# Kernel optimization log

Hardware: AMD Instinct MI355X
Metric: run time of the kernel (lower is better)

The kernel has to match this reference:

```python
import jax, jax.numpy as jnp
import numpy as np

UP = 16  # up_scale
EPS = 1e-5


def conv2d(x, w, b, pad):
    # x: [N,C,H,W], w: [O,I,kh,kw]
    out = jax.lax.conv_general_dilated(
        x, w, window_strides=(1, 1), padding=[(pad, pad), (pad, pad)],
        dimension_numbers=("NCHW", "OIHW", "NCHW"))
    return out + b[None, :, None, None]


def batchnorm(x, gamma, beta):
    # torch BatchNorm2d training mode: biased batch stats over (N,H,W)
    mu = jnp.mean(x, axis=(0, 2, 3), keepdims=True)
    var = jnp.var(x, axis=(0, 2, 3), keepdims=True)
    xn = (x - mu) * jax.lax.rsqrt(var + EPS)
    return xn * gamma[None, :, None, None] + beta[None, :, None, None]


def unfold3x3(x):
    # F.unfold(x, [3,3], padding=1) -> [N, C, 9, H, W] with (kh,kw) row-major order
    N, C, H, W = x.shape
    xp = jnp.pad(x, ((0, 0), (0, 0), (1, 1), (1, 1)))
    patches = [xp[:, :, i:i + H, j:j + W] for i in range(3) for j in range(3)]
    return jnp.stack(patches, axis=2)


def setup_inputs() -> dict:
    key = jax.random.key(0)
    ks = jax.random.split(key, 14)
    N, Cin, H, W = 4, 128, 64, 64
    Cout = 2
    s = 0.05
    inp = {
        "img_f": jax.random.normal(ks[0], (N, Cin, H, W), jnp.float32),
        # flowhead: conv3x3 -> BN -> ReLU -> conv3x3
        "fh_w1": jax.random.normal(ks[1], (Cout, Cin, 3, 3), jnp.float32) * s,
        "fh_b1": jax.random.normal(ks[2], (Cout,), jnp.float32) * s,
        "fh_g": jnp.ones((Cout,), jnp.float32),
        "fh_beta": jnp.zeros((Cout,), jnp.float32),
        "fh_w2": jax.random.normal(ks[3], (Cout, Cout, 3, 3), jnp.float32) * s,
        "fh_b2": jax.random.normal(ks[4], (Cout,), jnp.float32) * s,
        # mask head: conv3x3 -> BN -> ReLU -> conv1x1
        "mk_w1": jax.random.normal(ks[5], (UP * UP, Cin, 3, 3), jnp.float32) * s,
        "mk_b1": jax.random.normal(ks[6], (UP * UP,), jnp.float32) * s,
        "mk_g": jnp.ones((UP * UP,), jnp.float32),
        "mk_beta": jnp.zeros((UP * UP,), jnp.float32),
        "mk_w2": jax.random.normal(ks[7], (UP * UP * 9, UP * UP, 1, 1), jnp.float32) * s,
        "mk_b2": jax.random.normal(ks[8], (UP * UP * 9,), jnp.float32) * s,
    }
    return inp


def reference(img_f, fh_w1, fh_b1, fh_g, fh_beta, fh_w2, fh_b2,
              mk_w1, mk_b1, mk_g, mk_beta, mk_w2, mk_b2):
    # flow head
    h = conv2d(img_f, fh_w1, fh_b1, pad=1)
    h = jax.nn.relu(batchnorm(h, fh_g, fh_beta))
    flow = conv2d(h, fh_w2, fh_b2, pad=1)          # [N, C, H, W]

    # mask head
    m = conv2d(img_f, mk_w1, mk_b1, pad=1)
    m = jax.nn.relu(batchnorm(m, mk_g, mk_beta))
    mask = conv2d(m, mk_w2, mk_b2, pad=0) * 0.25   # [N, 9*UP*UP, H, W]

    N, C, H, W = flow.shape
    mask = mask.reshape(N, 1, 9, UP, UP, H, W)
    mask = jax.nn.softmax(mask, axis=2)

    up_flow = unfold3x3(8.0 * flow)                # [N, C, 9, H, W]
    up_flow = up_flow[:, :, :, None, None, :, :]   # [N, C, 9, 1, 1, H, W]
    up_flow = jnp.sum(mask * up_flow, axis=2)      # [N, C, UP, UP, H, W]
    up_flow = jnp.transpose(up_flow, (0, 1, 4, 2, 5, 3))  # [N, C, H, UP, W, UP]
    return up_flow.reshape(N, C, UP * H, UP * W)
```

## Files before the change

### kernel.cpp

```cpp
#include <hip/hip_runtime.h>
#include <hip/hip_bf16.h>

#define N_B   4
#define C_IN  128
#define HWSZ  4096
#define C_M   256

typedef __attribute__((ext_vector_type(8))) short          s16x8;
typedef __attribute__((ext_vector_type(8))) unsigned short u16x8;
typedef __attribute__((ext_vector_type(4))) unsigned short u16x4;
typedef __attribute__((ext_vector_type(4))) float          f32x4;

__device__ __forceinline__ unsigned short f2bf(float f) {
    union { float f; unsigned u; } v; v.f = f;
    unsigned r = v.u + 0x7fffu + ((v.u >> 16) & 1u);
    return (unsigned short)(r >> 16);
}
__device__ __forceinline__ float bf2f(unsigned short u) {
    union { unsigned u; float f; } v; v.u = ((unsigned)u) << 16; return v.f;
}

__global__ void __launch_bounds__(256)
prep_all(const float* __restrict__ img,
         const float* __restrict__ mk_w1, const float* __restrict__ fh_w1,
         const float* __restrict__ mk_w2,
         unsigned short* __restrict__ imgT,
         unsigned short* __restrict__ w1f, unsigned short* __restrict__ w2f)
{
    __shared__ float s[128][65];
    const int b = blockIdx.x;
    if (b < 256) {
        const int n = b >> 6, h = b & 63;
        const float* src = img + (size_t)n * C_IN * HWSZ + h * 64;
        for (int i = threadIdx.x; i < 128 * 64; i += 256) {
            int ci = i >> 6, w = i & 63;
            s[ci][w] = src[(size_t)ci * HWSZ + w];
        }
        __syncthreads();
        unsigned short* dst = imgT + ((size_t)(n * 64 + h) * 64) * 128;
        for (int i = threadIdx.x; i < 64 * 128; i += 256) {
            int w = i >> 7, ci = i & 127;
            dst[(size_t)w * 128 + ci] = f2bf(s[ci][w]);
        }
        return;
    }
    int i = (b - 256) * 256 + threadIdx.x;
    if (i < 2304 * 256) {
        int uvt = i / 36864;
        int r   = i - uvt * 36864;
        int k   = r / 4096;
        int r2  = r - k * 4096;
        int ks  = r2 >> 9;
        int lg  = (r2 >> 7) & 3;
        int ln  = (r2 >> 3) & 15;
        int j   = r2 & 7;
        w2f[i] = f2bf(0.25f * mk_w2[(size_t)(k * 256 + uvt * 16 + ln) * 256 + ks * 32 + lg * 8 + j]);
    }
    if (i < 2 * 4 * 9 * 9 * 512) {
        int z   = i / 165888;
        int r   = i - z * 165888;
        int cc  = r / 41472;
        int r2  = r - cc * 41472;
        int tap = r2 / 4608;
        int r3  = r2 - tap * 4608;
        int g   = r3 / 512;
        int r4  = r3 - g * 512;
        int lane = r4 >> 3, j = r4 & 7;
        int lg = lane >> 4, ln = lane & 15;
        int row = g * 16 + ln;
        int ci  = cc * 32 + lg * 8 + j;
        float w = 0.f;
        if (z == 0) {
            if (row < 128)      w = mk_w1[((size_t)row * C_IN + ci) * 9 + tap];
            else if (row < 130) w = fh_w1[((size_t)(row - 128) * C_IN + ci) * 9 + tap];
        } else {
            if (row < 128)      w = mk_w1[((size_t)(128 + row) * C_IN + ci) * 9 + tap];
        }
        w1f[i] = f2bf(w);
    }
}

__global__ void __launch_bounds__(512, 4)
conv1_mfma(const unsigned short* __restrict__ imgT,
           const unsigned short* __restrict__ w1f,
           const float* __restrict__ mk_b1, const float* __restrict__ fh_b1,
           unsigned short* __restrict__ m_frag, float* __restrict__ h_pre,
           float* __restrict__ ps_s, float* __restrict__ ps_s2)
{
    __shared__ unsigned short s_img[3][66][40];
    __shared__ float s_bias[144];
    __shared__ float s_ps[2][144], s_ps2[2][144];

    const int hw = blockIdx.x;
    const int xcd = hw & 7, slot = hw >> 3;
    const int lid = xcd * 64 + slot;
    const int n = lid >> 7, h = (lid >> 1) & 63, z = lid & 1;
    const int hn = n * 64 + h;

    const int tid = threadIdx.x;
    const int wv = tid >> 6, lane = tid & 63;
    const int lg = lane >> 4, ln = lane & 15;
    const int gq = wv >> 1, half = wv & 1;
    const int g0 = z ? (gq * 2) : ((int[4]){0, 3, 5, 7})[gq];
    const int gn = z ? 2 : ((int[4]){3, 2, 2, 2})[gq];

    if (tid < 144) {
        float b = 0.f;
        if (z == 0) {
            if (tid < 128)      b = mk_b1[tid];
            else if (tid < 130) b = fh_b1[tid - 128];
        } else if (tid < 128)   b = mk_b1[128 + tid];
        s_bias[tid] = b;
    }

    f32x4 acc[3][2];
#pragma unroll
    for (int g = 0; g < 3; ++g)
#pragma unroll
        for (int q = 0; q < 2; ++q) acc[g][q] = (f32x4){0.f, 0.f, 0.f, 0.f};

    for (int cc = 0; cc < 4; ++cc) {
        __syncthreads();
        for (int i = tid; i < 3 * 66 * 4; i += 512) {
            int r = i / 264;
            int rem = i - r * 264;
            int c = rem >> 2, un = rem & 3;
            int gy = h - 1 + r, gx = c - 1;
            u16x8 v = {0, 0, 0, 0, 0, 0, 0, 0};
            if ((unsigned)gy < 64u && (unsigned)gx < 64u)
                v = *(const u16x8*)&imgT[((size_t)((n * 64 + gy) * 64 + gx)) * 128 + cc * 32 + un * 8];
            *(u16x8*)&s_img[r][c][un * 8] = v;
        }
        __syncthreads();

        const unsigned short* wfp = w1f + (size_t)(z * 4 + cc) * 81 * 512 + lane * 8;
#pragma unroll
        for (int tap = 0; tap < 9; ++tap) {
            const int dy = tap / 3, dx = tap % 3;
            s16x8 bf[2];
#pragma unroll
            for (int q = 0; q < 2; ++q)
                bf[q] = *(const s16x8*)&s_img[dy][half * 32 + q * 16 + ln + dx][lg * 8];
#pragma unroll
            for (int gi = 0; gi < 3; ++gi) {
                if (gi < gn) {
                    s16x8 af = *(const s16x8*)&wfp[(size_t)(tap * 9 + g0 + gi) * 512];
#pragma unroll
                    for (int q = 0; q < 2; ++q)
                        acc[gi][q] = __builtin_amdgcn_mfma_f32_16x16x32_bf16(af, bf[q], acc[gi][q], 0, 0, 0);
                }
            }
        }
    }

#pragma unroll
    for (int gi = 0; gi < 3; ++gi) {
        if (gi >= gn) continue;
        const int g = g0 + gi;
        float v[2][4];
#pragma unroll
        for (int q = 0; q < 2; ++q)
#pragma unroll
            for (int r = 0; r < 4; ++r)
                v[q][r] = acc[gi][q][r] + s_bias[g * 16 + lg * 4 + r];
#pragma unroll
        for (int q = 0; q < 2; ++q) {
            const int px  = half * 32 + q * 16 + ln;
            const int pxg = h * 4 + half * 2 + q;
            if (z == 0 && g == 8) {
                if (lg == 0) {
#pragma unroll
                    for (int r = 0; r < 2; ++r)
                        h_pre[((size_t)(n * 2 + r)) * HWSZ + h * 64 + px] = v[q][r];
                }
            } else {
                u16x4 vv;
#pragma unroll
                for (int r = 0; r < 4; ++r) vv[r] = f2bf(v[q][r]);
                int ks  = z * 4 + (g >> 1);
                int lgp = ((g & 1) * 2 + (lg >> 1)) & 3;
                size_t off = ((((size_t)(n * 256 + pxg) * 8 + ks) * 4 + lgp) * 128) + ln * 8 + (lg & 1) * 4;
                *(u16x4*)&m_frag[off] = vv;
            }
        }
#pragma unroll
        for (int r = 0; r < 4; ++r) {
            float s  = v[0][r] + v[1][r];
            float s2 = v[0][r] * v[0][r] + v[1][r] * v[1][r];
#pragma unroll
            for (int off = 1; off < 16; off <<= 1) {
                s  += __shfl_xor(s,  off, 64);
                s2 += __shfl_xor(s2, off, 64);
            }
            if (ln == 0) {
                s_ps[half][g * 16 + lg * 4 + r]  = s;
                s_ps2[half][g * 16 + lg * 4 + r] = s2;
            }
        }
    }
    __syncthreads();
    const int nch = z ? 128 : 130;
    if (tid < nch) {
        const int idx = z * 146 + tid;
        ps_s[(size_t)idx * 256 + hn]  = s_ps[0][tid] + s_ps[1][tid];
        ps_s2[(size_t)idx * 256 + hn] = s_ps2[0][tid] + s_ps2[1][tid];
    }
}

__global__ void __launch_bounds__(64)
bn_final2(const float* __restrict__ ps_s, const float* __restrict__ ps_s2,
          const float* __restrict__ mk_g, const float* __restrict__ mk_be,
          const float* __restrict__ fh_g, const float* __restrict__ fh_be,
          float* __restrict__ ab_m, float* __restrict__ ab_h)
{
    const int b = blockIdx.x;
    const int idx = (b < 256) ? ((b >> 7) * 146 + (b & 127)) : (128 + (b - 256));
    const int t = threadIdx.x;
    float S = 0.f, S2 = 0.f;
    const float* p1 = ps_s  + (size_t)idx * 256;
    const float* p2 = ps_s2 + (size_t)idx * 256;
    for (int i = t; i < 256; i += 64) { S += p1[i]; S2 += p2[i]; }
#pragma unroll
    for (int off = 32; off > 0; off >>= 1) {
        S += __shfl_down(S, off, 64); S2 += __shfl_down(S2, off, 64);
    }
    if (t == 0) {
        const float inv = 1.0f / (float)(N_B * HWSZ);
        float mu = S * inv;
        float var = S2 * inv - mu * mu;
        float r = rsqrtf(var + 1e-5f);
        if (b < 256) {
            float a = mk_g[b] * r;
            ab_m[2 * b] = a; ab_m[2 * b + 1] = mk_be[b] - mu * a;
        } else {
            int c = b - 256;
            float a = fh_g[c] * r;
            ab_h[2 * c] = a; ab_h[2 * c + 1] = fh_be[c] - mu * a;
        }
    }
}

__global__ void __launch_bounds__(256)
bnrelu_flow(unsigned short* __restrict__ m_frag, const float* __restrict__ ab,
            const float* __restrict__ hpre, const float* __restrict__ ab_h,
            const float* __restrict__ w2, const float* __restrict__ b2,
            float* __restrict__ flow8)
{
    __shared__ float s_ab[512];
    const int t = threadIdx.x;
    if (blockIdx.x < 2048) {
        s_ab[t] = ab[t]; s_ab[256 + t] = ab[256 + t];
        __syncthreads();
        const unsigned u = blockIdx.x * 256 + t;
        const int lg = (u >> 4) & 3, ks = (u >> 7) & 7;
        const int cb = ks * 32 + lg * 8;
        u16x8 v = *(const u16x8*)&m_frag[(size_t)u * 8];
        u16x8 o;
#pragma unroll
        for (int j = 0; j < 8; ++j) {
            float a = s_ab[2 * (cb + j)], b = s_ab[2 * (cb + j) + 1];
            o[j] = f2bf(fmaxf(a * bf2f(v[j]) + b, 0.f));
        }
        *(u16x8*)&m_frag[(size_t)u * 8] = o;
        return;
    }
    int idx = (blockIdx.x - 2048) * 256 + t;
    int w = idx & 63, h = (idx >> 6) & 63, co = (idx >> 12) & 1, n = idx >> 13;
    float acc = b2[co];
#pragma unroll
    for (int ci = 0; ci < 2; ++ci) {
        float a = ab_h[2 * ci], b = ab_h[2 * ci + 1];
        const float* p = hpre + (size_t)(n * 2 + ci) * HWSZ;
        const float* wp = &w2[(co * 2 + ci) * 9];
#pragma unroll
        for (int dy = 0; dy < 3; ++dy)
#pragma unroll
            for (int dx = 0; dx < 3; ++dx) {
                int gy = h + dy - 1, gx = w + dx - 1;
                float v = 0.f;
                if ((unsigned)gy < 64u && (unsigned)gx < 64u)
                    v = fmaxf(a * p[gy * 64 + gx] + b, 0.f);
                acc += wp[dy * 3 + dx] * v;
            }
    }
    flow8[idx] = acc * 8.0f;
}

__global__ void __launch_bounds__(512, 4)
mask_combine_mfma(const unsigned short* __restrict__ m_frag,
                  const unsigned short* __restrict__ w2f,
                  const float* __restrict__ mk_b2,
                  const float* __restrict__ flow8,
                  float* __restrict__ out)
{
    __shared__ unsigned short s_w[36864];
    __shared__ float s_fl[2][6][66];
    __shared__ float s_bias[9][16];

    const int id = blockIdx.x;
    const int hg = id & 15, uvt = (id >> 4) & 15, n = id >> 8;

    const int tid = threadIdx.x;
    const int wv = tid >> 6, lane = tid & 63;
    const int lg = lane >> 4, ln = lane & 15;
    const int r_l = wv >> 1, half = wv & 1;
    const int h = hg * 4 + r_l;

    {
        const u16x8* wsrc = (const u16x8*)(w2f + (size_t)uvt * 36864);
        u16x8* wdst = (u16x8*)s_w;
        for (int i = tid; i < 4608; i += 512) wdst[i] = wsrc[i];
    }
    for (int i = tid; i < 2 * 6 * 66; i += 512) {
        int c = i / 396, rem = i - c * 396, r = rem / 66, col = rem - r * 66;
        int gy = hg * 4 - 1 + r, gx = col - 1;
        float v = 0.f;
        if ((unsigned)gy < 64u && (unsigned)gx < 64u)
            v = flow8[((size_t)(n * 2 + c)) * HWSZ + gy * 64 + gx];
        s_fl[c][r][col] = v;
    }
    if (tid < 144) s_bias[tid >> 4][tid & 15] = 0.25f * mk_b2[(tid >> 4) * 256 + uvt * 16 + (tid & 15)];
    __syncthreads();

    const unsigned short* wk0 = s_w + lg * 128 + ln * 8;
    const unsigned short* mb = m_frag + (size_t)(n * 256 + h * 4 + half * 2) * 4096 + lg * 128 + ln * 8;

    f32x4 acc[9][2];
#pragma unroll
    for (int k = 0; k < 9; ++k)
#pragma unroll
        for (int q = 0; q < 2; ++q) acc[k][q] = (f32x4){0.f, 0.f, 0.f, 0.f};

    s16x8 bq[2][2];
#pragma unroll
    for (int d = 0; d < 2; ++d)
#pragma unroll
        for (int q = 0; q < 2; ++q) bq[d][q] = *(const s16x8*)&mb[q * 4096 + d * 512];

#pragma unroll
    for (int ks = 0; ks < 8; ++ks) {
        const int d = ks & 1;
        const unsigned short* wk = wk0 + ks * 512;
#pragma unroll
        for (int k = 0; k < 9; ++k) {
            s16x8 af = *(const s16x8*)&wk[k * 4096];
#pragma unroll
            for (int q = 0; q < 2; ++q)
                acc[k][q] = __builtin_amdgcn_mfma_f32_16x16x32_bf16(af, bq[d][q], acc[k][q], 0, 0, 0);
        }
        if (ks < 6) {
#pragma unroll
            for (int q = 0; q < 2; ++q)
                bq[d][q] = *(const s16x8*)&mb[q * 4096 + (ks + 2) * 512];
        }
    }

    __syncthreads();
    float* s_o = (float*)s_w;

#pragma unroll
    for (int q = 0; q < 2; ++q) {
        const int w = half * 32 + q * 16 + ln;
        float o0[4], o1[4];
#pragma unroll
        for (int r = 0; r < 4; ++r) {
            const int vv = lg * 4 + r;
            float p[9], mx = -1e30f;
#pragma unroll
            for (int k = 0; k < 9; ++k) {
                p[k] = acc[k][q][r] + s_bias[k][vv];
                mx = fmaxf(mx, p[k]);
            }
            float sum = 0.f;
#pragma unroll
            for (int k = 0; k < 9; ++k) { p[k] = __expf(p[k] - mx); sum += p[k]; }
            float inv = 1.0f / sum;
            float a0 = 0.f, a1 = 0.f;
#pragma unroll
            for (int k = 0; k < 9; ++k) {
                const int dy = k / 3, dx = k % 3;
                a0 += p[k] * s_fl[0][r_l + dy][w + dx];
                a1 += p[k] * s_fl[1][r_l + dy][w + dx];
            }
            o0[r] = a0 * inv; o1[r] = a1 * inv;
        }
        *(f32x4*)&s_o[(0 * 4 + r_l) * 1024 + w * 16 + lg * 4] = (f32x4){o0[0], o0[1], o0[2], o0[3]};
        *(f32x4*)&s_o[(1 * 4 + r_l) * 1024 + w * 16 + lg * 4] = (f32x4){o1[0], o1[1], o1[2], o1[3]};
    }
    __syncthreads();

    for (int i = tid; i < 2048; i += 512) {
        const int idx = i * 4;
        const int row = idx >> 10;
        const int col = idx & 1023;
        const int c = row >> 2, rl = row & 3;
        f32x4 v = *(const f32x4*)&s_o[idx];
        *(f32x4*)(out + ((size_t)(n * 2 + c) * 1024 + (hg * 4 + rl) * 16 + uvt) * 1024 + col) = v;
    }
}

extern "C" void kernel_launch(void* const* d_in, const int* in_sizes, int n_in,
                              void* d_out, int out_size, void* d_ws, size_t ws_size,
                              hipStream_t stream) {
    const float* img   = (const float*)d_in[0];
    const float* fh_w1 = (const float*)d_in[1];
    const float* fh_b1 = (const float*)d_in[2];
    const float* fh_g  = (const float*)d_in[3];
    const float* fh_be = (const float*)d_in[4];
    const float* fh_w2 = (const float*)d_in[5];
    const float* fh_b2 = (const float*)d_in[6];
    const float* mk_w1 = (const float*)d_in[7];
    const float* mk_b1 = (const float*)d_in[8];
    const float* mk_g  = (const float*)d_in[9];
    const float* mk_be = (const float*)d_in[10];
    const float* mk_w2 = (const float*)d_in[11];
    const float* mk_b2 = (const float*)d_in[12];
    float* out = (float*)d_out;

    char* p = (char*)d_ws;
    unsigned short* w2f    = (unsigned short*)p;  p += (size_t)1179648;
    unsigned short* w1f    = (unsigned short*)p;  p += (size_t)663552;
    unsigned short* imgT   = (unsigned short*)p;  p += (size_t)4194304;
    unsigned short* m_frag = (unsigned short*)p;  p += (size_t)8388608;
    float* h_pre  = (float*)p;  p += (size_t)131072;
    float* flow8  = (float*)p;  p += (size_t)131072;
    float* ps_s   = (float*)p;  p += (size_t)280576;
    float* ps_s2  = (float*)p;  p += (size_t)280576;
    float* ab_m   = (float*)p;  p += 2048;
    float* ab_h   = (float*)p;  p += 64;

    prep_all<<<2560, 256, 0, stream>>>(img, mk_w1, fh_w1, mk_w2, imgT, w1f, w2f);
    conv1_mfma<<<512, 512, 0, stream>>>(imgT, w1f, mk_b1, fh_b1, m_frag, h_pre, ps_s, ps_s2);
    bn_final2<<<258, 64, 0, stream>>>(ps_s, ps_s2, mk_g, mk_be, fh_g, fh_be, ab_m, ab_h);
    bnrelu_flow<<<2176, 256, 0, stream>>>(m_frag, ab_m, h_pre, ab_h, fh_w2, fh_b2, flow8);
    mask_combine_mfma<<<1024, 512, 0, stream>>>(m_frag, w2f, mk_b2, flow8, out);
}
```

Baseline: 91.38 us.

## Double rows per block in mask combine kernel to amortize weight staging

The mask/combine kernel now processes 8 output rows per block instead of 4, using 1024 threads in 16 waves. Each wave handles one 16-column strip and loops over two passes. Halving the block count halves the repeated 72KB weight copy into LDS. The output staging buffer gets its own 32KB LDS array instead of aliasing the weight buffer. In exchange, LDS per block rises to about 110KB, which caps occupancy at one block per CU. Each wave also keeps fewer accumulators, and the two passes are serialized with extra barriers.

```diff
diff --git a/kernel.cpp b/kernel.cpp
--- a/kernel.cpp
+++ b/kernel.cpp
@@ -286,7 +286,7 @@
     flow8[idx] = acc * 8.0f;
 }
 
-__global__ void __launch_bounds__(512, 4)
+__global__ void __launch_bounds__(1024, 4)
 mask_combine_mfma(const unsigned short* __restrict__ m_frag,
                   const unsigned short* __restrict__ w2f,
                   const float* __restrict__ mk_b2,
@@ -294,26 +294,27 @@
                   float* __restrict__ out)
 {
     __shared__ unsigned short s_w[36864];
-    __shared__ float s_fl[2][6][66];
+    __shared__ float s_o[8192];
+    __shared__ float s_fl[2][10][66];
     __shared__ float s_bias[9][16];
 
     const int id = blockIdx.x;
-    const int hg = id & 15, uvt = (id >> 4) & 15, n = id >> 8;
+    const int hg = id & 7, uvt = (id >> 3) & 15, n = id >> 7;
 
     const int tid = threadIdx.x;
     const int wv = tid >> 6, lane = tid & 63;
     const int lg = lane >> 4, ln = lane & 15;
-    const int r_l = wv >> 1, half = wv & 1;
-    const int h = hg * 4 + r_l;
+    const int row_l = wv >> 2, qq = wv & 3;
+    const int w = qq * 16 + ln;
 
     {
         const u16x8* wsrc = (const u16x8*)(w2f + (size_t)uvt * 36864);
         u16x8* wdst = (u16x8*)s_w;
-        for (int i = tid; i < 4608; i += 512) wdst[i] = wsrc[i];
-    }
-    for (int i = tid; i < 2 * 6 * 66; i += 512) {
-        int c = i / 396, rem = i - c * 396, r = rem / 66, col = rem - r * 66;
-        int gy = hg * 4 - 1 + r, gx = col - 1;
+        for (int i = tid; i < 4608; i += 1024) wdst[i] = wsrc[i];
+    }
+    for (int i = tid; i < 2 * 10 * 66; i += 1024) {
+        int c = i / 660, rem = i - c * 660, r = rem / 66, col = rem - r * 66;
+        int gy = hg * 8 - 1 + r, gx = col - 1;
         float v = 0.f;
         if ((unsigned)gy < 64u && (unsigned)gx < 64u)
             v = flow8[((size_t)(n * 2 + c)) * HWSZ + gy * 64 + gx];
@@ -323,52 +324,38 @@
     __syncthreads();
 
     const unsigned short* wk0 = s_w + lg * 128 + ln * 8;
-    const unsigned short* mb = m_frag + (size_t)(n * 256 + h * 4 + half * 2) * 4096 + lg * 128 + ln * 8;
-
-    f32x4 acc[9][2];
-#pragma unroll
-    for (int k = 0; k < 9; ++k)
-#pragma unroll
-        for (int q = 0; q < 2; ++q) acc[k][q] = (f32x4){0.f, 0.f, 0.f, 0.f};
-
-    s16x8 bq[2][2];
-#pragma unroll
-    for (int d = 0; d < 2; ++d)
-#pragma unroll
-        for (int q = 0; q < 2; ++q) bq[d][q] = *(const s16x8*)&mb[q * 4096 + d * 512];
-
-#pragma unroll
-    for (int ks = 0; ks < 8; ++ks) {
-        const int d = ks & 1;
-        const unsigned short* wk = wk0 + ks * 512;
-#pragma unroll
-        for (int k = 0; k < 9; ++k) {
-            s16x8 af = *(const s16x8*)&wk[k * 4096];
-#pragma unroll
-            for (int q = 0; q < 2; ++q)
-                acc[k][q] = __builtin_amdgcn_mfma_f32_16x16x32_bf16(af, bq[d][q], acc[k][q], 0, 0, 0);
-        }
-        if (ks < 6) {
-#pragma unroll
-            for (int q = 0; q < 2; ++q)
-                bq[d][q] = *(const s16x8*)&mb[q * 4096 + (ks + 2) * 512];
-        }
-    }
-
-    __syncthreads();
-    float* s_o = (float*)s_w;
-
-#pragma unroll
-    for (int q = 0; q < 2; ++q) {
-        const int w = half * 32 + q * 16 + ln;
-        float o0[4], o1[4];
+
+    for (int pass = 0; pass < 2; ++pass) {
+        const int h = hg * 8 + pass * 4 + row_l;
+        const unsigned short* mb = m_frag + (size_t)(n * 256 + h * 4 + qq) * 4096 + lg * 128 + ln * 8;
+
+        f32x4 acc[9];
+#pragma unroll
+        for (int k = 0; k < 9; ++k) acc[k] = (f32x4){0.f, 0.f, 0.f, 0.f};
+
+        s16x8 bq[2];
+        bq[0] = *(const s16x8*)&mb[0];
+        bq[1] = *(const s16x8*)&mb[512];
+
+#pragma unroll
+        for (int ks = 0; ks < 8; ++ks) {
+            const int d = ks & 1;
+            const unsigned short* wk = wk0 + ks * 512;
+#pragma unroll
+            for (int k = 0; k < 9; ++k) {
+                s16x8 af = *(const s16x8*)&wk[k * 4096];
+                acc[k] = __builtin_amdgcn_mfma_f32_16x16x32_bf16(af, bq[d], acc[k], 0, 0, 0);
+            }
+            if (ks < 6) bq[d] = *(const s16x8*)&mb[(ks + 2) * 512];
+        }
+
 #pragma unroll
         for (int r = 0; r < 4; ++r) {
             const int vv = lg * 4 + r;
             float p[9], mx = -1e30f;
 #pragma unroll
             for (int k = 0; k < 9; ++k) {
-                p[k] = acc[k][q][r] + s_bias[k][vv];
+                p[k] = acc[k][r] + s_bias[k][vv];
                 mx = fmaxf(mx, p[k]);
             }
             float sum = 0.f;
@@ -379,23 +366,24 @@
 #pragma unroll
             for (int k = 0; k < 9; ++k) {
                 const int dy = k / 3, dx = k % 3;
-                a0 += p[k] * s_fl[0][r_l + dy][w + dx];
-                a1 += p[k] * s_fl[1][r_l + dy][w + dx];
-            }
-            o0[r] = a0 * inv; o1[r] = a1 * inv;
-        }
-        *(f32x4*)&s_o[(0 * 4 + r_l) * 1024 + w * 16 + lg * 4] = (f32x4){o0[0], o0[1], o0[2], o0[3]};
-        *(f32x4*)&s_o[(1 * 4 + r_l) * 1024 + w * 16 + lg * 4] = (f32x4){o1[0], o1[1], o1[2], o1[3]};
-    }
-    __syncthreads();
-
-    for (int i = tid; i < 2048; i += 512) {
-        const int idx = i * 4;
-        const int row = idx >> 10;
-        const int col = idx & 1023;
-        const int c = row >> 2, rl = row & 3;
-        f32x4 v = *(const f32x4*)&s_o[idx];
-        *(f32x4*)(out + ((size_t)(n * 2 + c) * 1024 + (hg * 4 + rl) * 16 + uvt) * 1024 + col) = v;
+                a0 += p[k] * s_fl[0][pass * 4 + row_l + dy][w + dx];
+                a1 += p[k] * s_fl[1][pass * 4 + row_l + dy][w + dx];
+            }
+            s_o[(0 * 4 + row_l) * 1024 + w * 16 + lg * 4 + r] = a0 * inv;
+            s_o[(1 * 4 + row_l) * 1024 + w * 16 + lg * 4 + r] = a1 * inv;
+        }
+        __syncthreads();
+
+        for (int i = tid; i < 2048; i += 1024) {
+            const int idx = i * 4;
+            const int row = idx >> 10;
+            const int col = idx & 1023;
+            const int c = row >> 2, rl = row & 3;
+            f32x4 v = *(const f32x4*)&s_o[idx];
+            *(f32x4*)(out + ((size_t)(n * 2 + c) * 1024 +
+                             (hg * 8 + pass * 4 + rl) * 16 + uvt) * 1024 + col) = v;
+        }
+        __syncthreads();
     }
 }
 
@@ -433,5 +421,5 @@
     conv1_mfma<<<512, 512, 0, stream>>>(imgT, w1f, mk_b1, fh_b1, m_frag, h_pre, ps_s, ps_s2);
     bn_final2<<<258, 64, 0, stream>>>(ps_s, ps_s2, mk_g, mk_be, fh_g, fh_be, ab_m, ab_h);
     bnrelu_flow<<<2176, 256, 0, stream>>>(m_frag, ab_m, h_pre, ab_h, fh_w2, fh_b2, flow8);
-    mask_combine_mfma<<<1024, 512, 0, stream>>>(m_frag, w2f, mk_b2, flow8, out);
-}
+    mask_combine_mfma<<<512, 1024, 0, stream>>>(m_frag, w2f, mk_b2, flow8, out);
+}
```

New measurement: 81.66 us. -10.6%, faster.

## Repack mask weights to 8 uv per block, pairing taps across lane halves

Applied to the files above, without the earlier changes.

The mask-combine kernel now handles 8 up-sampled positions per block instead of 16. Two softmax taps are packed into each MFMA row tile (10 padded taps in 5 tiles), so each wave issues 5 instead of 9 MFMA groups per k-step. The softmax and weighted flow sum are split across lane halves and combined with cross-lane shuffles, and output is stored directly without the shared-memory transpose. The costs are twice as many blocks re-reading m_frag, one wasted padded tap, and narrower direct stores.

```diff
diff --git a/kernel.cpp b/kernel.cpp
--- a/kernel.cpp
+++ b/kernel.cpp
@@ -45,16 +45,20 @@
         return;
     }
     int i = (b - 256) * 256 + threadIdx.x;
-    if (i < 2304 * 256) {
-        int uvt = i / 36864;
-        int r   = i - uvt * 36864;
-        int k   = r / 4096;
-        int r2  = r - k * 4096;
-        int ks  = r2 >> 9;
-        int lg  = (r2 >> 7) & 3;
-        int ln  = (r2 >> 3) & 15;
-        int j   = r2 & 7;
-        w2f[i] = f2bf(0.25f * mk_w2[(size_t)(k * 256 + uvt * 16 + ln) * 256 + ks * 32 + lg * 8 + j]);
+    if (i < 32 * 20480) {
+        int uvt8 = i / 20480;
+        int r    = i - uvt8 * 20480;
+        int t    = r / 4096;
+        int r2   = r - t * 4096;
+        int ks   = r2 >> 9;
+        int lane = (r2 >> 3) & 63;
+        int j    = r2 & 7;
+        int lg = lane >> 4, ln = lane & 15;
+        int k  = 2 * t + (ln >> 3);
+        int uv = uvt8 * 8 + (ln & 7);
+        int ci = ks * 32 + lg * 8 + j;
+        w2f[i] = (k < 9) ? f2bf(0.25f * mk_w2[(size_t)(k * 256 + uv) * 256 + ci])
+                         : (unsigned short)0;
     }
     if (i < 2 * 4 * 9 * 9 * 512) {
         int z   = i / 165888;
@@ -293,43 +297,47 @@
                   const float* __restrict__ flow8,
                   float* __restrict__ out)
 {
-    __shared__ unsigned short s_w[36864];
+    __shared__ unsigned short s_w[20480];
     __shared__ float s_fl[2][6][66];
-    __shared__ float s_bias[9][16];
+    __shared__ float s_bias[10][8];
 
     const int id = blockIdx.x;
-    const int hg = id & 15, uvt = (id >> 4) & 15, n = id >> 8;
+    const int hb = id & 15, uvt8 = (id >> 4) & 31, n = id >> 9;
 
     const int tid = threadIdx.x;
     const int wv = tid >> 6, lane = tid & 63;
     const int lg = lane >> 4, ln = lane & 15;
-    const int r_l = wv >> 1, half = wv & 1;
-    const int h = hg * 4 + r_l;
+    const int row_l = wv >> 1, half = wv & 1;
+    const int h = hb * 4 + row_l;
+    const int khalf = lg >> 1;
 
     {
-        const u16x8* wsrc = (const u16x8*)(w2f + (size_t)uvt * 36864);
+        const u16x8* wsrc = (const u16x8*)(w2f + (size_t)uvt8 * 20480);
         u16x8* wdst = (u16x8*)s_w;
-        for (int i = tid; i < 4608; i += 512) wdst[i] = wsrc[i];
+        for (int i = tid; i < 2560; i += 512) wdst[i] = wsrc[i];
     }
     for (int i = tid; i < 2 * 6 * 66; i += 512) {
         int c = i / 396, rem = i - c * 396, r = rem / 66, col = rem - r * 66;
-        int gy = hg * 4 - 1 + r, gx = col - 1;
+        int gy = hb * 4 - 1 + r, gx = col - 1;
         float v = 0.f;
         if ((unsigned)gy < 64u && (unsigned)gx < 64u)
             v = flow8[((size_t)(n * 2 + c)) * HWSZ + gy * 64 + gx];
         s_fl[c][r][col] = v;
     }
-    if (tid < 144) s_bias[tid >> 4][tid & 15] = 0.25f * mk_b2[(tid >> 4) * 256 + uvt * 16 + (tid & 15)];
+    if (tid < 80) {
+        int k = tid >> 3, uvl = tid & 7;
+        s_bias[k][uvl] = (k < 9) ? 0.25f * mk_b2[k * 256 + uvt8 * 8 + uvl] : -1e30f;
+    }
     __syncthreads();
 
     const unsigned short* wk0 = s_w + lg * 128 + ln * 8;
     const unsigned short* mb = m_frag + (size_t)(n * 256 + h * 4 + half * 2) * 4096 + lg * 128 + ln * 8;
 
-    f32x4 acc[9][2];
-#pragma unroll
-    for (int k = 0; k < 9; ++k)
-#pragma unroll
-        for (int q = 0; q < 2; ++q) acc[k][q] = (f32x4){0.f, 0.f, 0.f, 0.f};
+    f32x4 acc[5][2];
+#pragma unroll
+    for (int t = 0; t < 5; ++t)
+#pragma unroll
+        for (int q = 0; q < 2; ++q) acc[t][q] = (f32x4){0.f, 0.f, 0.f, 0.f};
 
     s16x8 bq[2][2];
 #pragma unroll
@@ -340,13 +348,12 @@
 #pragma unroll
     for (int ks = 0; ks < 8; ++ks) {
         const int d = ks & 1;
-        const unsigned short* wk = wk0 + ks * 512;
-#pragma unroll
-        for (int k = 0; k < 9; ++k) {
-            s16x8 af = *(const s16x8*)&wk[k * 4096];
+#pragma unroll
+        for (int t = 0; t < 5; ++t) {
+            s16x8 af = *(const s16x8*)&wk0[(t * 8 + ks) * 512];
 #pragma unroll
             for (int q = 0; q < 2; ++q)
-                acc[k][q] = __builtin_amdgcn_mfma_f32_16x16x32_bf16(af, bq[d][q], acc[k][q], 0, 0, 0);
+                acc[t][q] = __builtin_amdgcn_mfma_f32_16x16x32_bf16(af, bq[d][q], acc[t][q], 0, 0, 0);
         }
         if (ks < 6) {
 #pragma unroll
@@ -355,47 +362,43 @@
         }
     }
 
-    __syncthreads();
-    float* s_o = (float*)s_w;
+    const int dyE[5] = {0, 0, 1, 2, 2}, dxE[5] = {0, 2, 1, 0, 2};
+    const int dyO[5] = {0, 1, 1, 2, 2}, dxO[5] = {1, 0, 2, 1, 2};
 
 #pragma unroll
     for (int q = 0; q < 2; ++q) {
-        const int w = half * 32 + q * 16 + ln;
-        float o0[4], o1[4];
+        const int wpx = half * 32 + q * 16 + ln;
+        float o[4];
 #pragma unroll
         for (int r = 0; r < 4; ++r) {
-            const int vv = lg * 4 + r;
-            float p[9], mx = -1e30f;
-#pragma unroll
-            for (int k = 0; k < 9; ++k) {
-                p[k] = acc[k][q][r] + s_bias[k][vv];
-                mx = fmaxf(mx, p[k]);
-            }
-            float sum = 0.f;
-#pragma unroll
-            for (int k = 0; k < 9; ++k) { p[k] = __expf(p[k] - mx); sum += p[k]; }
-            float inv = 1.0f / sum;
+            const int uvl = (lg & 1) * 4 + r;
+            float v5[5], mx = -1e30f;
+#pragma unroll
+            for (int t = 0; t < 5; ++t) {
+                v5[t] = acc[t][q][r] + s_bias[2 * t + khalf][uvl];
+                mx = fmaxf(mx, v5[t]);
+            }
+            mx = fmaxf(mx, __shfl_xor(mx, 32, 64));
+            float p5[5], s5 = 0.f;
+#pragma unroll
+            for (int t = 0; t < 5; ++t) { p5[t] = __expf(v5[t] - mx); s5 += p5[t]; }
+            float sum = s5 + __shfl_xor(s5, 32, 64);
             float a0 = 0.f, a1 = 0.f;
 #pragma unroll
-            for (int k = 0; k < 9; ++k) {
-                const int dy = k / 3, dx = k % 3;
-                a0 += p[k] * s_fl[0][r_l + dy][w + dx];
-                a1 += p[k] * s_fl[1][r_l + dy][w + dx];
-            }
-            o0[r] = a0 * inv; o1[r] = a1 * inv;
-        }
-        *(f32x4*)&s_o[(0 * 4 + r_l) * 1024 + w * 16 + lg * 4] = (f32x4){o0[0], o0[1], o0[2], o0[3]};
-        *(f32x4*)&s_o[(1 * 4 + r_l) * 1024 + w * 16 + lg * 4] = (f32x4){o1[0], o1[1], o1[2], o1[3]};
-    }
-    __syncthreads();
-
-    for (int i = tid; i < 2048; i += 512) {
-        const int idx = i * 4;
-        const int row = idx >> 10;
-        const int col = idx & 1023;
-        const int c = row >> 2, rl = row & 3;
-        f32x4 v = *(const f32x4*)&s_o[idx];
-        *(f32x4*)(out + ((size_t)(n * 2 + c) * 1024 + (hg * 4 + rl) * 16 + uvt) * 1024 + col) = v;
+            for (int t = 0; t < 5; ++t) {
+                const int dy = khalf ? dyO[t] : dyE[t];
+                const int dx = khalf ? dxO[t] : dxE[t];
+                a0 += p5[t] * s_fl[0][row_l + dy][wpx + dx];
+                a1 += p5[t] * s_fl[1][row_l + dy][wpx + dx];
+            }
+            a0 += __shfl_xor(a0, 32, 64);
+            a1 += __shfl_xor(a1, 32, 64);
+            const float inv = 1.0f / sum;
+            o[r] = (khalf ? a1 : a0) * inv;
+        }
+        float* base = out + ((size_t)(n * 2 + khalf) * 1024 + h * 16 + (uvt8 >> 1)) * 1024
+                      + wpx * 16 + (uvt8 & 1) * 8 + (lg & 1) * 4;
+        *(f32x4*)base = (f32x4){o[0], o[1], o[2], o[3]};
     }
 }
 
@@ -418,7 +421,7 @@
     float* out = (float*)d_out;
 
     char* p = (char*)d_ws;
-    unsigned short* w2f    = (unsigned short*)p;  p += (size_t)1179648;
+    unsigned short* w2f    = (unsigned short*)p;  p += (size_t)1310720;
     unsigned short* w1f    = (unsigned short*)p;  p += (size_t)663552;
     unsigned short* imgT   = (unsigned short*)p;  p += (size_t)4194304;
     unsigned short* m_frag = (unsigned short*)p;  p += (size_t)8388608;
@@ -429,9 +432,9 @@
     float* ab_m   = (float*)p;  p += 2048;
     float* ab_h   = (float*)p;  p += 64;
 
-    prep_all<<<2560, 256, 0, stream>>>(img, mk_w1, fh_w1, mk_w2, imgT, w1f, w2f);
+    prep_all<<<2816, 256, 0, stream>>>(img, mk_w1, fh_w1, mk_w2, imgT, w1f, w2f);
     conv1_mfma<<<512, 512, 0, stream>>>(imgT, w1f, mk_b1, fh_b1, m_frag, h_pre, ps_s, ps_s2);
     bn_final2<<<258, 64, 0, stream>>>(ps_s, ps_s2, mk_g, mk_be, fh_g, fh_be, ab_m, ab_h);
     bnrelu_flow<<<2176, 256, 0, stream>>>(m_frag, ab_m, h_pre, ab_h, fh_w2, fh_b2, flow8);
-    mask_combine_mfma<<<1024, 512, 0, stream>>>(m_frag, w2f, mk_b2, flow8, out);
-}
+    mask_combine_mfma<<<2048, 512, 0, stream>>>(m_frag, w2f, mk_b2, flow8, out);
+}
```

Measured after the change: 84.62 us. 1.08x faster.
